# Kernel tuning notes

Hardware: AMD Instinct MI355X
Metric: run time of the kernel (lower is better)

Reference implementation:

```python
import jax, jax.numpy as jnp
import numpy as np

B, N = 8, 2048
CLIP, D, BD, NC = 512, 256, 128, 10  # CLIP_EMBED_DIM, GNN_NODE_DIM, BOTTLENECK_DIM_GNN, NUM_CLASSES
LN_EPS = 1e-5


def _layer_norm(x, g, b):
    mu = jnp.mean(x, axis=-1, keepdims=True)
    var = jnp.mean(jnp.square(x - mu), axis=-1, keepdims=True)
    return (x - mu) / jnp.sqrt(var + LN_EPS) * g + b


def setup_inputs() -> dict:
    key = jax.random.key(0)
    ks = jax.random.split(key, 16)
    def w(k, shape, fan_in):
        lim = 1.0 / np.sqrt(fan_in)
        return jax.random.uniform(k, shape, jnp.float32, -lim, lim)
    return {
        "local_feat": jax.random.normal(ks[0], (B, N, CLIP), jnp.float32),
        "coords": jax.random.uniform(ks[1], (B, N, 2), jnp.float32),
        "mask": jax.random.randint(ks[2], (B, N), 0, 2).astype(bool),
        # node_encoder: Linear(CLIP->D) + LayerNorm(D)
        "enc_w": w(ks[3], (CLIP, D), CLIP), "enc_b": jnp.zeros((D,), jnp.float32),
        "enc_g": jnp.ones((D,), jnp.float32), "enc_beta": jnp.zeros((D,), jnp.float32),
        "gamma": jnp.asarray(5.0, jnp.float32),  # spatial_gamma
        "wq": w(ks[4], (D, D), D), "bq": jnp.zeros((D,), jnp.float32),
        "wk": w(ks[5], (D, D), D), "bk": jnp.zeros((D,), jnp.float32),
        "wv": w(ks[6], (D, D), D), "bv": jnp.zeros((D,), jnp.float32),
        # bottleneck: Linear(D->BD) + LayerNorm(BD)
        "bn_w": w(ks[7], (D, BD), D), "bn_b": jnp.zeros((BD,), jnp.float32),
        "bn_g": jnp.ones((BD,), jnp.float32), "bn_beta": jnp.zeros((BD,), jnp.float32),
        # classifier: Linear(BD->BD//2) + ReLU + Linear(BD//2->NC)
        "c1_w": w(ks[8], (BD, BD // 2), BD), "c1_b": jnp.zeros((BD // 2,), jnp.float32),
        "c2_w": w(ks[9], (BD // 2, NC), BD // 2), "c2_b": jnp.zeros((NC,), jnp.float32),
    }


def reference(local_feat, coords, mask, enc_w, enc_b, enc_g, enc_beta, gamma,
              wq, bq, wk, bk, wv, bv, bn_w, bn_b, bn_g, bn_beta,
              c1_w, c1_b, c2_w, c2_b):
    # node encoder: Linear + LN + ReLU -> h [B,N,D]
    h = jax.nn.relu(_layer_norm(local_feat @ enc_w + enc_b, enc_g, enc_beta))
    # pairwise euclidean distances on 2D coords (torch.cdist, under no_grad)
    xy = coords[:, :, :2]
    sq = jnp.sum(xy * xy, axis=-1)                                   # [B,N]
    d2 = sq[:, :, None] + sq[:, None, :] - 2.0 * jnp.einsum('bnd,bmd->bnm', xy, xy)
    dist = jax.lax.stop_gradient(jnp.sqrt(jnp.maximum(d2, 0.0)))     # [B,N,N]
    spatial_adj = jnp.exp(-dist * jnp.abs(gamma))
    q, k, v = h @ wq + bq, h @ wk + bk, h @ wv + bv
    scores = jnp.einsum('bnd,bmd->bnm', q, k) / jnp.sqrt(jnp.float32(D))
    attn = jax.nn.softmax(scores, axis=-1) * spatial_adj             # gated attention
    attn = jnp.where(mask[:, None, :], 0.0, attn)                    # zero masked keys
    agg = jnp.einsum('bnm,bmd->bnd', attn, v)                        # [B,N,D]
    out = jax.nn.relu(_layer_norm(agg @ bn_w + bn_b, bn_g, bn_beta)) # [B,N,BD]
    mask_v = (~mask)[:, :, None].astype(out.dtype)                   # [B,N,1]
    pooled = (out * mask_v).sum(axis=1) / jnp.maximum(mask_v.sum(axis=1), 1e-9)
    logits = jax.nn.relu(pooled @ c1_w + c1_b) @ c2_w + c2_b
    return logits, pooled
```

## Files before the change

kernel.cpp:

```cpp
#include <hip/hip_runtime.h>
#include <hip/hip_bf16.h>

typedef unsigned short ushort_t;
typedef __attribute__((ext_vector_type(8))) short s8;
typedef __attribute__((ext_vector_type(4))) float f4;

__device__ __forceinline__ unsigned short f2bf(float f) {
  union { float f; unsigned int u; } c; c.f = f;
  unsigned int r = (c.u + 0x7fffu + ((c.u >> 16) & 1u)) >> 16;
  return (unsigned short)r;
}
__device__ __forceinline__ float bf2f(ushort_t u) {
  union { unsigned int i; float f; } c; c.i = ((unsigned int)u) << 16; return c.f;
}
__device__ __forceinline__ uint4 pack8(float4 a, float4 b) {
  uint4 r;
  r.x = (unsigned)f2bf(a.x) | ((unsigned)f2bf(a.y) << 16);
  r.y = (unsigned)f2bf(a.z) | ((unsigned)f2bf(a.w) << 16);
  r.z = (unsigned)f2bf(b.x) | ((unsigned)f2bf(b.y) << 16);
  r.w = (unsigned)f2bf(b.z) | ((unsigned)f2bf(b.w) << 16);
  return r;
}
__device__ __forceinline__ float fsqrt_fast(float x) {
  float r; asm("v_sqrt_f32 %0, %1" : "=v"(r) : "v"(x)); return r;
}
__device__ __forceinline__ float fexp2_fast(float x) {
  float r; asm("v_exp_f32 %0, %1" : "=v"(r) : "v"(x)); return r;
}
__device__ __forceinline__ void dma16(const ushort_t* g, const short* l) {
  __builtin_amdgcn_global_load_lds(
      (const __attribute__((address_space(1))) unsigned int*)g,
      (__attribute__((address_space(3))) unsigned int*)(unsigned long)l,
      16, 0, 0);
}

#define LOG2E 1.44269504f

__global__ __launch_bounds__(256) void k_wt_all(
    const float* __restrict__ enc_w, const float* __restrict__ wq,
    const float* __restrict__ wk, const float* __restrict__ wv,
    const float* __restrict__ bn_w, const int* __restrict__ mask,
    ushort_t* __restrict__ enc_wT, ushort_t* __restrict__ wqkvT,
    ushort_t* __restrict__ bn_wT, float* __restrict__ pooledAcc) {
  const int y = blockIdx.y;
  const int i = blockIdx.x * 256 + threadIdx.x;
  if (y == 0) {
    if (i < 131072) { const int n = i >> 9, k = i & 511; enc_wT[i] = f2bf(enc_w[k * 256 + n]); }
  } else if (y <= 3) {
    if (i < 65536) {
      const int n = i >> 8, k = i & 255;
      const float* src = (y == 1) ? wq : (y == 2) ? wk : wv;
      wqkvT[(y - 1) * 65536 + i] = f2bf(src[k * 256 + n]);
    }
  } else if (y == 4) {
    if (i < 32768) { const int n = i >> 8, k = i & 255; bn_wT[i] = f2bf(bn_w[k * 128 + n]); }
  } else {
    if (i < 16384) pooledAcc[1024 + i] = mask[i] ? 0.f : 1.f;
    if (i < 1024) pooledAcc[i] = 0.f;
  }
}

__global__ __launch_bounds__(256, 3) void k_gemm_enc(
    const float* __restrict__ A, const ushort_t* __restrict__ WT,
    const float* __restrict__ bia, const float* __restrict__ g,
    const float* __restrict__ beta, ushort_t* __restrict__ out) {
  __shared__ short Al[32 * 72];
  __shared__ short Bl[256 * 72];
  __shared__ float red1[32][2], red2[32][2];
  const int t = threadIdx.x;
  const int wv = t >> 6, lane = t & 63, l16 = lane & 15, quad = lane >> 4;
  const int wm = wv >> 1, wn = wv & 1;
  const int row0 = blockIdx.x * 32;

  f4 acc[8];
#pragma unroll
  for (int nf = 0; nf < 8; ++nf) acc[nf] = (f4){0.f, 0.f, 0.f, 0.f};

  for (int k0 = 0; k0 < 512; k0 += 64) {
    __syncthreads();
    {
      const int r = t >> 3, c8 = t & 7;
      const float* src = &A[(size_t)(row0 + r) * 512 + k0 + c8 * 8];
      *(uint4*)&Al[r * 72 + c8 * 8] =
          pack8(*(const float4*)src, *(const float4*)(src + 4));
    }
#pragma unroll
    for (int i = 0; i < 8; ++i) {
      const int ch = t + i * 256;
      const int r = ch >> 3, c8 = ch & 7;
      *(uint4*)&Bl[r * 72 + c8 * 8] =
          *(const uint4*)&WT[(size_t)r * 512 + k0 + c8 * 8];
    }
    __syncthreads();
#pragma unroll
    for (int kc = 0; kc < 2; ++kc) {
      const s8 af = *(const s8*)&Al[(wm * 16 + l16) * 72 + kc * 32 + quad * 8];
#pragma unroll
      for (int nf = 0; nf < 8; ++nf) {
        const s8 bf = *(const s8*)&Bl[(wn * 128 + nf * 16 + l16) * 72 + kc * 32 + quad * 8];
        acc[nf] = __builtin_amdgcn_mfma_f32_16x16x32_bf16(af, bf, acc[nf], 0, 0, 0);
      }
    }
  }
  float bi[8], gg[8], bb[8];
#pragma unroll
  for (int nf = 0; nf < 8; ++nf) {
    const int col = wn * 128 + nf * 16 + l16;
    bi[nf] = bia[col]; gg[nf] = g[col]; bb[nf] = beta[col];
  }
  float s1[4] = {0.f, 0.f, 0.f, 0.f}, s2[4] = {0.f, 0.f, 0.f, 0.f};
#pragma unroll
  for (int nf = 0; nf < 8; ++nf)
#pragma unroll
    for (int r = 0; r < 4; ++r) {
      const float v = acc[nf][r] + bi[nf];
      acc[nf][r] = v;
      s1[r] += v; s2[r] += v * v;
    }
#pragma unroll
  for (int m = 1; m < 16; m <<= 1) {
#pragma unroll
    for (int r = 0; r < 4; ++r) {
      s1[r] += __shfl_xor(s1[r], m);
      s2[r] += __shfl_xor(s2[r], m);
    }
  }
  if (l16 == 0) {
#pragma unroll
    for (int r = 0; r < 4; ++r) {
      const int rl = wm * 16 + quad * 4 + r;
      red1[rl][wn] = s1[r]; red2[rl][wn] = s2[r];
    }
  }
  __syncthreads();
#pragma unroll
  for (int r = 0; r < 4; ++r) {
    const int rl = wm * 16 + quad * 4 + r;
    const float mu = (red1[rl][0] + red1[rl][1]) * (1.f / 256.f);
    const float var = (red2[rl][0] + red2[rl][1]) * (1.f / 256.f) - mu * mu;
    const float rstd = rsqrtf(var + 1e-5f);
#pragma unroll
    for (int nf = 0; nf < 8; ++nf) {
      const int col = wn * 128 + nf * 16 + l16;
      const float v = (acc[nf][r] - mu) * rstd * gg[nf] + bb[nf];
      out[(size_t)(row0 + rl) * 256 + col] = f2bf(fmaxf(v, 0.f));
    }
  }
}

__global__ __launch_bounds__(256, 3) void k_gemm_qkv(
    const ushort_t* __restrict__ A, const ushort_t* __restrict__ WT,
    const float* __restrict__ bq, const float* __restrict__ bk,
    const float* __restrict__ bv,
    ushort_t* __restrict__ q, ushort_t* __restrict__ k, ushort_t* __restrict__ vt) {
  __shared__ short Al[64 * 72];
  __shared__ short Bl[256 * 72];
  const int t = threadIdx.x;
  const int wv = t >> 6, lane = t & 63, l16 = lane & 15, quad = lane >> 4;
  const int wm = wv >> 1, wn = wv & 1;
  const int row0 = blockIdx.x * 64;
  const int type = blockIdx.y;
  const ushort_t* wtb = WT + (size_t)type * 65536;

  f4 acc[2][8];
#pragma unroll
  for (int mf = 0; mf < 2; ++mf)
#pragma unroll
    for (int nf = 0; nf < 8; ++nf) acc[mf][nf] = (f4){0.f, 0.f, 0.f, 0.f};

  for (int k0 = 0; k0 < 256; k0 += 64) {
    __syncthreads();
#pragma unroll
    for (int i = 0; i < 2; ++i) {
      const int ch = t + i * 256;
      const int r = ch >> 3, c8 = ch & 7;
      *(uint4*)&Al[r * 72 + c8 * 8] =
          *(const uint4*)&A[(size_t)(row0 + r) * 256 + k0 + c8 * 8];
    }
#pragma unroll
    for (int i = 0; i < 8; ++i) {
      const int ch = t + i * 256;
      const int r = ch >> 3, c8 = ch & 7;
      *(uint4*)&Bl[r * 72 + c8 * 8] =
          *(const uint4*)&wtb[(size_t)r * 256 + k0 + c8 * 8];
    }
    __syncthreads();
#pragma unroll
    for (int kc = 0; kc < 2; ++kc) {
      s8 af[2];
      af[0] = *(const s8*)&Al[(wm * 32 + l16) * 72 + kc * 32 + quad * 8];
      af[1] = *(const s8*)&Al[(wm * 32 + 16 + l16) * 72 + kc * 32 + quad * 8];
#pragma unroll
      for (int nf = 0; nf < 8; ++nf) {
        const s8 bf = *(const s8*)&Bl[(wn * 128 + nf * 16 + l16) * 72 + kc * 32 + quad * 8];
        acc[0][nf] = __builtin_amdgcn_mfma_f32_16x16x32_bf16(af[0], bf, acc[0][nf], 0, 0, 0);
        acc[1][nf] = __builtin_amdgcn_mfma_f32_16x16x32_bf16(af[1], bf, acc[1][nf], 0, 0, 0);
      }
    }
  }
  const float* bias = (type == 0) ? bq : (type == 1) ? bk : bv;
#pragma unroll
  for (int nf = 0; nf < 8; ++nf) {
    const int col = wn * 128 + nf * 16 + l16;
    const float bi = bias[col];
    if (type == 2) {
      const int b = row0 >> 11;
#pragma unroll
      for (int mf = 0; mf < 2; ++mf) {
        const int n = (row0 & 2047) + wm * 32 + quad * 8 + mf * 4;
        ushort4 pk;
        pk.x = f2bf(acc[mf][nf][0] + bi);
        pk.y = f2bf(acc[mf][nf][1] + bi);
        pk.z = f2bf(acc[mf][nf][2] + bi);
        pk.w = f2bf(acc[mf][nf][3] + bi);
        *(ushort4*)&vt[((size_t)b * 256 + col) * 2048 + n] = pk;
      }
    } else {
      ushort_t* dst = (type == 0) ? q : k;
      const float sc = (type == 0) ? (0.0625f * LOG2E) : 1.f;
#pragma unroll
      for (int mf = 0; mf < 2; ++mf)
#pragma unroll
        for (int r = 0; r < 4; ++r) {
          const int row = row0 + wm * 32 + mf * 16 + quad * 4 + r;
          dst[(size_t)row * 256 + col] = f2bf((acc[mf][nf][r] + bi) * sc);
        }
    }
  }
}

__global__ __launch_bounds__(512, 2) void k_attn(
    const ushort_t* __restrict__ qb, const ushort_t* __restrict__ kb,
    const ushort_t* __restrict__ vtb,
    const float* __restrict__ coords, const int* __restrict__ mask,
    const float* __restrict__ gam,
    ushort_t* __restrict__ Opb, float* __restrict__ lws) {
  __shared__ short kld[3][8192];
  __shared__ short vld[3][8192];
  __shared__ __align__(16) float2 cls[512];
  __shared__ __align__(16) float  mls[512];
  const int t = threadIdx.x;
  const int wv = t >> 6, lane = t & 63, l16 = lane & 15, quad = lane >> 4;
  const int b = blockIdx.z, ks = blockIdx.y;
  const int qw = blockIdx.x * 256 + wv * 32;
  const int kbase = ks * 512;

  const ushort_t* kbb = kb + ((size_t)b * 2048 + kbase) * 256;
  const ushort_t* vbb = vtb + (size_t)b * 256 * 2048 + kbase;

  auto stage = [&](int tt, int ib) {
    const ushort_t* kn = kbb + (size_t)tt * 8192;
    const ushort_t* vn = vbb + tt * 32;
    const int key = t & 31, dg = t >> 5;
    dma16(kn + (size_t)key * 256 + dg * 8, &kld[ib][t * 8]);
    dma16(kn + (size_t)key * 256 + dg * 8 + 128, &kld[ib][(t + 512) * 8]);
    const int d = t & 255, kg = t >> 8;
    dma16(vn + (size_t)d * 2048 + kg * 8, &vld[ib][t * 8]);
    dma16(vn + (size_t)d * 2048 + kg * 8 + 16, &vld[ib][(t + 512) * 8]);
  };

  stage(0, 0);
  stage(1, 1);
  cls[t] = ((const float2*)coords)[b * 2048 + kbase + t];
  mls[t] = mask[b * 2048 + kbase + t] ? 0.f : 1.f;

  s8 qa[2][8];
  {
    const ushort_t* qrow = qb + ((size_t)b * 2048 + qw + l16) * 256 + quad * 8;
#pragma unroll
    for (int c = 0; c < 8; ++c) {
      qa[0][c] = *(const s8*)(qrow + c * 32);
      qa[1][c] = *(const s8*)(qrow + 16 * 256 + c * 32);
    }
  }
  float rcx[2], rcy[2];
  {
    const float2 c0 = ((const float2*)coords)[b * 2048 + qw + l16];
    const float2 c1 = ((const float2*)coords)[b * 2048 + qw + 16 + l16];
    rcx[0] = c0.x; rcy[0] = c0.y; rcx[1] = c1.x; rcy[1] = c1.y;
  }
  const float gl2 = fabsf(gam[0]) * LOG2E;

  f4 o[2][16];
#pragma unroll
  for (int h = 0; h < 2; ++h)
#pragma unroll
    for (int dt = 0; dt < 16; ++dt) o[h][dt] = (f4){0.f, 0.f, 0.f, 0.f};
  float lrun[2] = {0.f, 0.f};

  auto compute_tile = [&](int kt, const short* kldc, const short* vldc) {
    f4 sc[2][2];
    sc[0][0] = (f4){0.f, 0.f, 0.f, 0.f}; sc[0][1] = (f4){0.f, 0.f, 0.f, 0.f};
    sc[1][0] = (f4){0.f, 0.f, 0.f, 0.f}; sc[1][1] = (f4){0.f, 0.f, 0.f, 0.f};
#pragma unroll
    for (int c = 0; c < 8; ++c) {
      const s8 kf0 = *(const s8*)&kldc[((c * 4 + quad) * 32 + l16) * 8];
      sc[0][0] = __builtin_amdgcn_mfma_f32_16x16x32_bf16(kf0, qa[0][c], sc[0][0], 0, 0, 0);
      sc[1][0] = __builtin_amdgcn_mfma_f32_16x16x32_bf16(kf0, qa[1][c], sc[1][0], 0, 0, 0);
      const s8 kf1 = *(const s8*)&kldc[((c * 4 + quad) * 32 + 16 + l16) * 8];
      sc[0][1] = __builtin_amdgcn_mfma_f32_16x16x32_bf16(kf1, qa[0][c], sc[0][1], 0, 0, 0);
      sc[1][1] = __builtin_amdgcn_mfma_f32_16x16x32_bf16(kf1, qa[1][c], sc[1][1], 0, 0, 0);
    }
    s8 paf[2];
#pragma unroll
    for (int h = 0; h < 2; ++h) {
      unsigned pu[4];
#pragma unroll
      for (int s = 0; s < 2; ++s) {
        const int k0 = kt * 32 + s * 16 + quad * 4;
        const float4 c01 = *(const float4*)&cls[k0];
        const float4 c23 = *(const float4*)&cls[k0 + 2];
        const float4 mm = *(const float4*)&mls[k0];
        const float kx[4] = {c01.x, c01.z, c23.x, c23.z};
        const float ky[4] = {c01.y, c01.w, c23.y, c23.w};
        const float mv[4] = {mm.x, mm.y, mm.z, mm.w};
        float w[4];
#pragma unroll
        for (int r = 0; r < 4; ++r) {
          const float p = fexp2_fast(sc[h][s][r]);
          lrun[h] += p;
          const float dx = rcx[h] - kx[r], dy = rcy[h] - ky[r];
          const float dist = fsqrt_fast(dx * dx + dy * dy);
          w[r] = p * fexp2_fast(-gl2 * dist) * mv[r];
        }
        pu[s * 2 + 0] = (unsigned)f2bf(w[0]) | ((unsigned)f2bf(w[1]) << 16);
        pu[s * 2 + 1] = (unsigned)f2bf(w[2]) | ((unsigned)f2bf(w[3]) << 16);
      }
      union { s8 v; unsigned u[4]; } cv;
      cv.u[0] = pu[0]; cv.u[1] = pu[1]; cv.u[2] = pu[2]; cv.u[3] = pu[3];
      paf[h] = cv.v;
    }
#pragma unroll
    for (int dt = 0; dt < 16; ++dt) {
      const s8 bvf = *(const s8*)&vldc[(quad * 256 + dt * 16 + l16) * 8];
      o[0][dt] = __builtin_amdgcn_mfma_f32_16x16x32_bf16(paf[0], bvf, o[0][dt], 0, 0, 0);
      o[1][dt] = __builtin_amdgcn_mfma_f32_16x16x32_bf16(paf[1], bvf, o[1][dt], 0, 0, 0);
    }
  };

  __syncthreads();
  stage(2, 2);
  compute_tile(0, kld[0], vld[0]);

  int cur = 1;
  for (int kt = 1; kt < 15; ++kt) {
    asm volatile("s_waitcnt vmcnt(4)" ::: "memory");
    __builtin_amdgcn_s_barrier();
    __builtin_amdgcn_sched_barrier(0);
    const int nb3 = (cur + 2 >= 3) ? cur - 1 : cur + 2;
    stage(kt + 2, nb3);
    compute_tile(kt, kld[cur], vld[cur]);
    cur = (cur + 1 >= 3) ? 0 : cur + 1;
  }
  asm volatile("s_waitcnt vmcnt(0)" ::: "memory");
  __builtin_amdgcn_s_barrier();
  __builtin_amdgcn_sched_barrier(0);
  compute_tile(15, kld[cur], vld[cur]);

  ushort_t* OpK = Opb + (size_t)ks * 4194304;
#pragma unroll
  for (int h = 0; h < 2; ++h)
#pragma unroll
    for (int dt = 0; dt < 16; ++dt)
#pragma unroll
      for (int r = 0; r < 4; ++r)
        OpK[((size_t)b * 2048 + qw + h * 16 + quad * 4 + r) * 256 + dt * 16 + l16] =
            f2bf(o[h][dt][r]);

#pragma unroll
  for (int h = 0; h < 2; ++h) {
    lrun[h] += __shfl_xor(lrun[h], 16);
    lrun[h] += __shfl_xor(lrun[h], 32);
  }
  if (quad == 0) {
    lws[ks * 16384 + b * 2048 + qw + l16] = lrun[0];
    lws[ks * 16384 + b * 2048 + qw + 16 + l16] = lrun[1];
  }
}

__global__ __launch_bounds__(256, 3) void k_gemm_bn(
    const ushort_t* __restrict__ Opb, const float* __restrict__ lws,
    const ushort_t* __restrict__ WT,
    const float* __restrict__ bia, const float* __restrict__ g,
    const float* __restrict__ beta, float* __restrict__ pooledAcc) {
  __shared__ short Al[32 * 72];
  __shared__ short Bl[128 * 72];
  __shared__ float red1[32][2], red2[32][2];
  __shared__ float sCm[32];
  const int t = threadIdx.x;
  const int wv = t >> 6, lane = t & 63, l16 = lane & 15, quad = lane >> 4;
  const int wm = wv >> 1, wn = wv & 1;
  const int row0 = blockIdx.x * 32;
  const int b = row0 >> 11;

  if (t < 32) {
    const int row = row0 + t;
    sCm[t] = 1.f / (lws[row] + lws[16384 + row] + lws[32768 + row] + lws[49152 + row]);
  }

  f4 acc[4];
#pragma unroll
  for (int nf = 0; nf < 4; ++nf) acc[nf] = (f4){0.f, 0.f, 0.f, 0.f};

  for (int k0 = 0; k0 < 256; k0 += 64) {
    __syncthreads();
    {
      const int r = t >> 3, c8 = t & 7;
      const float c0 = sCm[r];
      const size_t off = (size_t)(row0 + r) * 256 + k0 + c8 * 8;
      float e[8];
#pragma unroll
      for (int j = 0; j < 8; ++j) e[j] = 0.f;
#pragma unroll
      for (int pp = 0; pp < 4; ++pp) {
        const uint4 u = *(const uint4*)&Opb[(size_t)pp * 4194304 + off];
        e[0] += bf2f((ushort_t)(u.x & 0xffff)); e[1] += bf2f((ushort_t)(u.x >> 16));
        e[2] += bf2f((ushort_t)(u.y & 0xffff)); e[3] += bf2f((ushort_t)(u.y >> 16));
        e[4] += bf2f((ushort_t)(u.z & 0xffff)); e[5] += bf2f((ushort_t)(u.z >> 16));
        e[6] += bf2f((ushort_t)(u.w & 0xffff)); e[7] += bf2f((ushort_t)(u.w >> 16));
      }
      float4 ea = {c0 * e[0], c0 * e[1], c0 * e[2], c0 * e[3]};
      float4 eb = {c0 * e[4], c0 * e[5], c0 * e[6], c0 * e[7]};
      *(uint4*)&Al[r * 72 + c8 * 8] = pack8(ea, eb);
    }
#pragma unroll
    for (int i = 0; i < 4; ++i) {
      const int ch = t + i * 256;
      const int r = ch >> 3, c8 = ch & 7;
      *(uint4*)&Bl[r * 72 + c8 * 8] =
          *(const uint4*)&WT[(size_t)r * 256 + k0 + c8 * 8];
    }
    __syncthreads();
#pragma unroll
    for (int kc = 0; kc < 2; ++kc) {
      const s8 af = *(const s8*)&Al[(wm * 16 + l16) * 72 + kc * 32 + quad * 8];
#pragma unroll
      for (int nf = 0; nf < 4; ++nf) {
        const s8 bf = *(const s8*)&Bl[(wn * 64 + nf * 16 + l16) * 72 + kc * 32 + quad * 8];
        acc[nf] = __builtin_amdgcn_mfma_f32_16x16x32_bf16(af, bf, acc[nf], 0, 0, 0);
      }
    }
  }
  float bi[4], gg[4], bb[4];
#pragma unroll
  for (int nf = 0; nf < 4; ++nf) {
    const int col = wn * 64 + nf * 16 + l16;
    bi[nf] = bia[col]; gg[nf] = g[col]; bb[nf] = beta[col];
  }
  float s1[4] = {0.f, 0.f, 0.f, 0.f}, s2[4] = {0.f, 0.f, 0.f, 0.f};
#pragma unroll
  for (int nf = 0; nf < 4; ++nf)
#pragma unroll
    for (int r = 0; r < 4; ++r) {
      const float v = acc[nf][r] + bi[nf];
      acc[nf][r] = v;
      s1[r] += v; s2[r] += v * v;
    }
#pragma unroll
  for (int m = 1; m < 16; m <<= 1) {
#pragma unroll
    for (int r = 0; r < 4; ++r) {
      s1[r] += __shfl_xor(s1[r], m);
      s2[r] += __shfl_xor(s2[r], m);
    }
  }
  if (l16 == 0) {
#pragma unroll
    for (int r = 0; r < 4; ++r) {
      const int rl = wm * 16 + quad * 4 + r;
      red1[rl][wn] = s1[r]; red2[rl][wn] = s2[r];
    }
  }
  __syncthreads();
#pragma unroll
  for (int r = 0; r < 4; ++r) {
    const int rl = wm * 16 + quad * 4 + r;
    const float mu = (red1[rl][0] + red1[rl][1]) * (1.f / 128.f);
    const float var = (red2[rl][0] + red2[rl][1]) * (1.f / 128.f) - mu * mu;
    const float rstd = rsqrtf(var + 1e-5f);
#pragma unroll
    for (int nf = 0; nf < 4; ++nf) {
      const float v = (acc[nf][r] - mu) * rstd * gg[nf] + bb[nf];
      acc[nf][r] = fmaxf(v, 0.f);
    }
  }
  {
    float mw[4];
#pragma unroll
    for (int r = 0; r < 4; ++r) {
      const int rl = wm * 16 + quad * 4 + r;
      mw[r] = pooledAcc[1024 + row0 + rl];
    }
#pragma unroll
    for (int nf = 0; nf < 4; ++nf) {
      float s = acc[nf][0] * mw[0] + acc[nf][1] * mw[1] +
                acc[nf][2] * mw[2] + acc[nf][3] * mw[3];
      s += __shfl_xor(s, 16);
      s += __shfl_xor(s, 32);
      if (quad == 0) {
        const int col = wn * 64 + nf * 16 + l16;
        atomicAdd(&pooledAcc[b * 128 + col], s);
      }
    }
  }
}

__global__ __launch_bounds__(128) void k_pool2_head(
    const float* __restrict__ pooledAcc, const int* __restrict__ mask,
    const float* __restrict__ c1w, const float* __restrict__ c1b,
    const float* __restrict__ c2w, const float* __restrict__ c2b,
    float* __restrict__ dout) {
  __shared__ float ps[128];
  __shared__ float h1[64];
  __shared__ float scnt[128];
  const int b = blockIdx.x, t = threadIdx.x;
  float c = 0.f;
  const int* mb = mask + b * 2048 + t * 16;
#pragma unroll
  for (int j = 0; j < 16; ++j) c += mb[j] ? 0.f : 1.f;
  scnt[t] = c;
  __syncthreads();
  for (int o2 = 64; o2 > 0; o2 >>= 1) {
    if (t < o2) scnt[t] += scnt[t + o2];
    __syncthreads();
  }
  const float cnt = scnt[0];
  const float p = pooledAcc[b * 128 + t] / fmaxf(cnt, 1e-9f);
  ps[t] = p;
  dout[80 + b * 128 + t] = p;
  __syncthreads();
  if (t < 64) {
    float acc = c1b[t];
    for (int d = 0; d < 128; ++d) acc += ps[d] * c1w[d * 64 + t];
    h1[t] = fmaxf(acc, 0.f);
  }
  __syncthreads();
  if (t < 10) {
    float a2 = c2b[t];
    for (int j = 0; j < 64; ++j) a2 += h1[j] * c2w[j * 10 + t];
    dout[b * 10 + t] = a2;
  }
}

extern "C" void kernel_launch(void* const* d_in, const int* in_sizes, int n_in,
                              void* d_out, int out_size, void* d_ws, size_t ws_size,
                              hipStream_t stream) {
  const float* lf     = (const float*)d_in[0];
  const float* coords = (const float*)d_in[1];
  const int*   mask   = (const int*)d_in[2];
  const float* enc_w  = (const float*)d_in[3];
  const float* enc_b  = (const float*)d_in[4];
  const float* enc_g  = (const float*)d_in[5];
  const float* enc_be = (const float*)d_in[6];
  const float* gamma  = (const float*)d_in[7];
  const float* wq     = (const float*)d_in[8];
  const float* bq     = (const float*)d_in[9];
  const float* wk     = (const float*)d_in[10];
  const float* bk     = (const float*)d_in[11];
  const float* wv     = (const float*)d_in[12];
  const float* bv     = (const float*)d_in[13];
  const float* bn_w   = (const float*)d_in[14];
  const float* bn_b   = (const float*)d_in[15];
  const float* bn_g   = (const float*)d_in[16];
  const float* bn_be  = (const float*)d_in[17];
  const float* c1w    = (const float*)d_in[18];
  const float* c1b    = (const float*)d_in[19];
  const float* c2w    = (const float*)d_in[20];
  const float* c2b    = (const float*)d_in[21];

  float* ws = (float*)d_ws;
  ushort_t* h_bf   = (ushort_t*)ws;
  ushort_t* q_bf   = (ushort_t*)(ws + 2097152);
  ushort_t* k_bf   = (ushort_t*)(ws + 4194304);
  ushort_t* vt_bf  = (ushort_t*)(ws + 6291456);
  ushort_t* Opb    = (ushort_t*)(ws + 8388608);
  ushort_t* enc_wT = (ushort_t*)(ws + 17825792);
  ushort_t* wqkvT  = (ushort_t*)(ws + 17891328);
  ushort_t* bn_wT  = (ushort_t*)(ws + 17989632);
  float*    lws    = ws + 18006016;
  float*    pooledAcc = ws + 18071552;
  float* out = (float*)d_out;

  k_wt_all<<<dim3(512, 6), 256, 0, stream>>>(enc_w, wq, wk, wv, bn_w, mask,
                                             enc_wT, wqkvT, bn_wT, pooledAcc);
  k_gemm_enc<<<512, 256, 0, stream>>>(lf, enc_wT, enc_b, enc_g, enc_be, h_bf);
  k_gemm_qkv<<<dim3(256, 3), 256, 0, stream>>>(h_bf, wqkvT, bq, bk, bv, q_bf, k_bf, vt_bf);
  k_attn<<<dim3(8, 4, 8), 512, 0, stream>>>(q_bf, k_bf, vt_bf, coords, mask, gamma,
                                            Opb, lws);
  k_gemm_bn<<<512, 256, 0, stream>>>(Opb, lws, bn_wT, bn_b, bn_g, bn_be, pooledAcc);
  k_pool2_head<<<8, 128, 0, stream>>>(pooledAcc, mask, c1w, c1b, c2w, c2b, out);
}
```

Before: 215.2 us.

## Fuse node encoder GEMM+LayerNorm with QKV projection, keeping h in LDS

```diff
diff --git a/kernel.cpp b/kernel.cpp
--- a/kernel.cpp
+++ b/kernel.cpp
@@ -60,171 +60,154 @@
   }
 }
 
-__global__ __launch_bounds__(256, 3) void k_gemm_enc(
+__global__ __launch_bounds__(256, 2) void k_enc_qkv(
     const float* __restrict__ A, const ushort_t* __restrict__ WT,
     const float* __restrict__ bia, const float* __restrict__ g,
-    const float* __restrict__ beta, ushort_t* __restrict__ out) {
+    const float* __restrict__ beta,
+    const ushort_t* __restrict__ WQKV,
+    const float* __restrict__ bq, const float* __restrict__ bk,
+    const float* __restrict__ bv,
+    ushort_t* __restrict__ q, ushort_t* __restrict__ kko, ushort_t* __restrict__ vt) {
   __shared__ short Al[32 * 72];
   __shared__ short Bl[256 * 72];
+  __shared__ short hl[32 * 264];
   __shared__ float red1[32][2], red2[32][2];
   const int t = threadIdx.x;
   const int wv = t >> 6, lane = t & 63, l16 = lane & 15, quad = lane >> 4;
   const int wm = wv >> 1, wn = wv & 1;
   const int row0 = blockIdx.x * 32;
 
-  f4 acc[8];
-#pragma unroll
-  for (int nf = 0; nf < 8; ++nf) acc[nf] = (f4){0.f, 0.f, 0.f, 0.f};
-
-  for (int k0 = 0; k0 < 512; k0 += 64) {
+  {
+    f4 acc[8];
+#pragma unroll
+    for (int nf = 0; nf < 8; ++nf) acc[nf] = (f4){0.f, 0.f, 0.f, 0.f};
+
+    for (int k0 = 0; k0 < 512; k0 += 64) {
+      __syncthreads();
+      {
+        const int r = t >> 3, c8 = t & 7;
+        const float* src = &A[(size_t)(row0 + r) * 512 + k0 + c8 * 8];
+        *(uint4*)&Al[r * 72 + c8 * 8] =
+            pack8(*(const float4*)src, *(const float4*)(src + 4));
+      }
+#pragma unroll
+      for (int i = 0; i < 8; ++i) {
+        const int ch = t + i * 256;
+        const int r = ch >> 3, c8 = ch & 7;
+        *(uint4*)&Bl[r * 72 + c8 * 8] =
+            *(const uint4*)&WT[(size_t)r * 512 + k0 + c8 * 8];
+      }
+      __syncthreads();
+#pragma unroll
+      for (int kc = 0; kc < 2; ++kc) {
+        const s8 af = *(const s8*)&Al[(wm * 16 + l16) * 72 + kc * 32 + quad * 8];
+#pragma unroll
+        for (int nf = 0; nf < 8; ++nf) {
+          const s8 bf = *(const s8*)&Bl[(wn * 128 + nf * 16 + l16) * 72 + kc * 32 + quad * 8];
+          acc[nf] = __builtin_amdgcn_mfma_f32_16x16x32_bf16(af, bf, acc[nf], 0, 0, 0);
+        }
+      }
+    }
+    float bi[8], gg[8], bb[8];
+#pragma unroll
+    for (int nf = 0; nf < 8; ++nf) {
+      const int col = wn * 128 + nf * 16 + l16;
+      bi[nf] = bia[col]; gg[nf] = g[col]; bb[nf] = beta[col];
+    }
+    float s1[4] = {0.f, 0.f, 0.f, 0.f}, s2[4] = {0.f, 0.f, 0.f, 0.f};
+#pragma unroll
+    for (int nf = 0; nf < 8; ++nf)
+#pragma unroll
+      for (int r = 0; r < 4; ++r) {
+        const float v = acc[nf][r] + bi[nf];
+        acc[nf][r] = v;
+        s1[r] += v; s2[r] += v * v;
+      }
+#pragma unroll
+    for (int m = 1; m < 16; m <<= 1) {
+#pragma unroll
+      for (int r = 0; r < 4; ++r) {
+        s1[r] += __shfl_xor(s1[r], m);
+        s2[r] += __shfl_xor(s2[r], m);
+      }
+    }
+    if (l16 == 0) {
+#pragma unroll
+      for (int r = 0; r < 4; ++r) {
+        const int rl = wm * 16 + quad * 4 + r;
+        red1[rl][wn] = s1[r]; red2[rl][wn] = s2[r];
+      }
+    }
     __syncthreads();
-    {
-      const int r = t >> 3, c8 = t & 7;
-      const float* src = &A[(size_t)(row0 + r) * 512 + k0 + c8 * 8];
-      *(uint4*)&Al[r * 72 + c8 * 8] =
-          pack8(*(const float4*)src, *(const float4*)(src + 4));
-    }
-#pragma unroll
-    for (int i = 0; i < 8; ++i) {
-      const int ch = t + i * 256;
-      const int r = ch >> 3, c8 = ch & 7;
-      *(uint4*)&Bl[r * 72 + c8 * 8] =
-          *(const uint4*)&WT[(size_t)r * 512 + k0 + c8 * 8];
-    }
-    __syncthreads();
-#pragma unroll
-    for (int kc = 0; kc < 2; ++kc) {
-      const s8 af = *(const s8*)&Al[(wm * 16 + l16) * 72 + kc * 32 + quad * 8];
-#pragma unroll
-      for (int nf = 0; nf < 8; ++nf) {
-        const s8 bf = *(const s8*)&Bl[(wn * 128 + nf * 16 + l16) * 72 + kc * 32 + quad * 8];
-        acc[nf] = __builtin_amdgcn_mfma_f32_16x16x32_bf16(af, bf, acc[nf], 0, 0, 0);
-      }
-    }
-  }
-  float bi[8], gg[8], bb[8];
-#pragma unroll
-  for (int nf = 0; nf < 8; ++nf) {
-    const int col = wn * 128 + nf * 16 + l16;
-    bi[nf] = bia[col]; gg[nf] = g[col]; bb[nf] = beta[col];
-  }
-  float s1[4] = {0.f, 0.f, 0.f, 0.f}, s2[4] = {0.f, 0.f, 0.f, 0.f};
-#pragma unroll
-  for (int nf = 0; nf < 8; ++nf)
-#pragma unroll
-    for (int r = 0; r < 4; ++r) {
-      const float v = acc[nf][r] + bi[nf];
-      acc[nf][r] = v;
-      s1[r] += v; s2[r] += v * v;
-    }
-#pragma unroll
-  for (int m = 1; m < 16; m <<= 1) {
-#pragma unroll
-    for (int r = 0; r < 4; ++r) {
-      s1[r] += __shfl_xor(s1[r], m);
-      s2[r] += __shfl_xor(s2[r], m);
-    }
-  }
-  if (l16 == 0) {
 #pragma unroll
     for (int r = 0; r < 4; ++r) {
       const int rl = wm * 16 + quad * 4 + r;
-      red1[rl][wn] = s1[r]; red2[rl][wn] = s2[r];
-    }
-  }
-  __syncthreads();
-#pragma unroll
-  for (int r = 0; r < 4; ++r) {
-    const int rl = wm * 16 + quad * 4 + r;
-    const float mu = (red1[rl][0] + red1[rl][1]) * (1.f / 256.f);
-    const float var = (red2[rl][0] + red2[rl][1]) * (1.f / 256.f) - mu * mu;
-    const float rstd = rsqrtf(var + 1e-5f);
-#pragma unroll
-    for (int nf = 0; nf < 8; ++nf) {
-      const int col = wn * 128 + nf * 16 + l16;
-      const float v = (acc[nf][r] - mu) * rstd * gg[nf] + bb[nf];
-      out[(size_t)(row0 + rl) * 256 + col] = f2bf(fmaxf(v, 0.f));
-    }
-  }
-}
-
-__global__ __launch_bounds__(256, 3) void k_gemm_qkv(
-    const ushort_t* __restrict__ A, const ushort_t* __restrict__ WT,
-    const float* __restrict__ bq, const float* __restrict__ bk,
-    const float* __restrict__ bv,
-    ushort_t* __restrict__ q, ushort_t* __restrict__ k, ushort_t* __restrict__ vt) {
-  __shared__ short Al[64 * 72];
-  __shared__ short Bl[256 * 72];
-  const int t = threadIdx.x;
-  const int wv = t >> 6, lane = t & 63, l16 = lane & 15, quad = lane >> 4;
-  const int wm = wv >> 1, wn = wv & 1;
-  const int row0 = blockIdx.x * 64;
-  const int type = blockIdx.y;
-  const ushort_t* wtb = WT + (size_t)type * 65536;
-
-  f4 acc[2][8];
-#pragma unroll
-  for (int mf = 0; mf < 2; ++mf)
-#pragma unroll
-    for (int nf = 0; nf < 8; ++nf) acc[mf][nf] = (f4){0.f, 0.f, 0.f, 0.f};
-
-  for (int k0 = 0; k0 < 256; k0 += 64) {
-    __syncthreads();
-#pragma unroll
-    for (int i = 0; i < 2; ++i) {
-      const int ch = t + i * 256;
-      const int r = ch >> 3, c8 = ch & 7;
-      *(uint4*)&Al[r * 72 + c8 * 8] =
-          *(const uint4*)&A[(size_t)(row0 + r) * 256 + k0 + c8 * 8];
-    }
-#pragma unroll
-    for (int i = 0; i < 8; ++i) {
-      const int ch = t + i * 256;
-      const int r = ch >> 3, c8 = ch & 7;
-      *(uint4*)&Bl[r * 72 + c8 * 8] =
-          *(const uint4*)&wtb[(size_t)r * 256 + k0 + c8 * 8];
-    }
-    __syncthreads();
-#pragma unroll
-    for (int kc = 0; kc < 2; ++kc) {
-      s8 af[2];
-      af[0] = *(const s8*)&Al[(wm * 32 + l16) * 72 + kc * 32 + quad * 8];
-      af[1] = *(const s8*)&Al[(wm * 32 + 16 + l16) * 72 + kc * 32 + quad * 8];
+      const float mu = (red1[rl][0] + red1[rl][1]) * (1.f / 256.f);
+      const float var = (red2[rl][0] + red2[rl][1]) * (1.f / 256.f) - mu * mu;
+      const float rstd = rsqrtf(var + 1e-5f);
 #pragma unroll
       for (int nf = 0; nf < 8; ++nf) {
-        const s8 bf = *(const s8*)&Bl[(wn * 128 + nf * 16 + l16) * 72 + kc * 32 + quad * 8];
-        acc[0][nf] = __builtin_amdgcn_mfma_f32_16x16x32_bf16(af[0], bf, acc[0][nf], 0, 0, 0);
-        acc[1][nf] = __builtin_amdgcn_mfma_f32_16x16x32_bf16(af[1], bf, acc[1][nf], 0, 0, 0);
-      }
-    }
-  }
-  const float* bias = (type == 0) ? bq : (type == 1) ? bk : bv;
-#pragma unroll
-  for (int nf = 0; nf < 8; ++nf) {
-    const int col = wn * 128 + nf * 16 + l16;
-    const float bi = bias[col];
+        const int col = wn * 128 + nf * 16 + l16;
+        const float v = (acc[nf][r] - mu) * rstd * gg[nf] + bb[nf];
+        hl[rl * 264 + col] = (short)f2bf(fmaxf(v, 0.f));
+      }
+    }
+  }
+
+  const int b = row0 >> 11;
+  for (int type = 0; type < 3; ++type) {
+    const ushort_t* wtb = WQKV + (size_t)type * 65536;
+    f4 acc[8];
+#pragma unroll
+    for (int nf = 0; nf < 8; ++nf) acc[nf] = (f4){0.f, 0.f, 0.f, 0.f};
+
+    for (int k0 = 0; k0 < 256; k0 += 64) {
+      __syncthreads();
+#pragma unroll
+      for (int i = 0; i < 8; ++i) {
+        const int ch = t + i * 256;
+        const int r = ch >> 3, c8 = ch & 7;
+        *(uint4*)&Bl[r * 72 + c8 * 8] =
+            *(const uint4*)&wtb[(size_t)r * 256 + k0 + c8 * 8];
+      }
+      __syncthreads();
+#pragma unroll
+      for (int kc = 0; kc < 2; ++kc) {
+        const s8 af = *(const s8*)&hl[(wm * 16 + l16) * 264 + k0 + kc * 32 + quad * 8];
+#pragma unroll
+        for (int nf = 0; nf < 8; ++nf) {
+          const s8 bf = *(const s8*)&Bl[(wn * 128 + nf * 16 + l16) * 72 + kc * 32 + quad * 8];
+          acc[nf] = __builtin_amdgcn_mfma_f32_16x16x32_bf16(af, bf, acc[nf], 0, 0, 0);
+        }
+      }
+    }
+    const float* bias = (type == 0) ? bq : (type == 1) ? bk : bv;
     if (type == 2) {
-      const int b = row0 >> 11;
-#pragma unroll
-      for (int mf = 0; mf < 2; ++mf) {
-        const int n = (row0 & 2047) + wm * 32 + quad * 8 + mf * 4;
+#pragma unroll
+      for (int nf = 0; nf < 8; ++nf) {
+        const int col = wn * 128 + nf * 16 + l16;
+        const float bi = bias[col];
+        const int n = (row0 & 2047) + quad * 8 + wm * 4;
         ushort4 pk;
-        pk.x = f2bf(acc[mf][nf][0] + bi);
-        pk.y = f2bf(acc[mf][nf][1] + bi);
-        pk.z = f2bf(acc[mf][nf][2] + bi);
-        pk.w = f2bf(acc[mf][nf][3] + bi);
+        pk.x = f2bf(acc[nf][0] + bi);
+        pk.y = f2bf(acc[nf][1] + bi);
+        pk.z = f2bf(acc[nf][2] + bi);
+        pk.w = f2bf(acc[nf][3] + bi);
         *(ushort4*)&vt[((size_t)b * 256 + col) * 2048 + n] = pk;
       }
     } else {
-      ushort_t* dst = (type == 0) ? q : k;
+      ushort_t* dst = (type == 0) ? q : kko;
       const float sc = (type == 0) ? (0.0625f * LOG2E) : 1.f;
 #pragma unroll
-      for (int mf = 0; mf < 2; ++mf)
+      for (int nf = 0; nf < 8; ++nf) {
+        const int col = wn * 128 + nf * 16 + l16;
+        const float bi = bias[col];
 #pragma unroll
         for (int r = 0; r < 4; ++r) {
-          const int row = row0 + wm * 32 + mf * 16 + quad * 4 + r;
-          dst[(size_t)row * 256 + col] = f2bf((acc[mf][nf][r] + bi) * sc);
+          const int row = row0 + wm * 16 + quad * 4 + r;
+          dst[(size_t)row * 256 + col] = f2bf((acc[nf][r] + bi) * sc);
         }
+      }
     }
   }
 }
@@ -569,7 +552,6 @@
   const float* c2b    = (const float*)d_in[21];
 
   float* ws = (float*)d_ws;
-  ushort_t* h_bf   = (ushort_t*)ws;
   ushort_t* q_bf   = (ushort_t*)(ws + 2097152);
   ushort_t* k_bf   = (ushort_t*)(ws + 4194304);
   ushort_t* vt_bf  = (ushort_t*)(ws + 6291456);
@@ -583,8 +565,8 @@
 
   k_wt_all<<<dim3(512, 6), 256, 0, stream>>>(enc_w, wq, wk, wv, bn_w, mask,
                                              enc_wT, wqkvT, bn_wT, pooledAcc);
-  k_gemm_enc<<<512, 256, 0, stream>>>(lf, enc_wT, enc_b, enc_g, enc_be, h_bf);
-  k_gemm_qkv<<<dim3(256, 3), 256, 0, stream>>>(h_bf, wqkvT, bq, bk, bv, q_bf, k_bf, vt_bf);
+  k_enc_qkv<<<512, 256, 0, stream>>>(lf, enc_wT, enc_b, enc_g, enc_be,
+                                     wqkvT, bq, bk, bv, q_bf, k_bf, vt_bf);
   k_attn<<<dim3(8, 4, 8), 512, 0, stream>>>(q_bf, k_bf, vt_bf, coords, mask, gamma,
                                             Opb, lws);
   k_gemm_bn<<<512, 256, 0, stream>>>(Opb, lws, bn_wT, bn_b, bn_g, bn_be, pooledAcc);
```

Result: slower. 220.7 us (+2.5%).
